# Kernel optimization log

Hardware: AMD Instinct MI355X
Metric: run time of the kernel (lower is better)

## Reference

```python
import jax, jax.numpy as jnp
import numpy as np

N, NOBJ, M, H, W = 512, 16, 8192, 128, 128


def _rand_rotations(key, n):
    A = jax.random.normal(key, (n, 3, 3), dtype=jnp.float32)
    q, r = jnp.linalg.qr(A)
    q = q * jnp.sign(jnp.diagonal(r, axis1=-2, axis2=-1))[:, None, :]
    det = jnp.linalg.det(q)  # +-1; flip first column if det == -1
    q = q.at[:, :, 0].multiply(det[:, None])
    return q


def setup_inputs() -> dict:
    key = jax.random.key(0)
    ks = jax.random.split(key, 10)
    obj_id = jax.random.randint(ks[0], (N,), 0, NOBJ, dtype=jnp.int32)
    # realistic pinhole intrinsics (pixels), slight per-sample jitter
    base_K = jnp.array([[600.0, 0.0, 64.0], [0.0, 600.0, 64.0], [0.0, 0.0, 1.0]], jnp.float32)
    cam_K = base_K[None] + jax.random.normal(ks[1], (N, 3, 3)) * jnp.array(
        [[5.0, 0.0, 1.0], [0.0, 5.0, 1.0], [0.0, 0.0, 0.0]], jnp.float32)
    gt_R = _rand_rotations(ks[2], N)
    # small rotational perturbation for pred
    pred_R = _rand_rotations(ks[3], N) @ gt_R
    gt_t = jnp.concatenate([jax.random.normal(ks[4], (N, 2)) * 20.0,
                            500.0 + jax.random.uniform(ks[4], (N, 1)) * 300.0], axis=-1)
    pred_t = gt_t + jax.random.normal(ks[5], (N, 3)) * 5.0
    mesh_points = jax.random.normal(ks[6], (NOBJ, M, 3)) * 50.0  # mm-scale meshes
    diameters = 150.0 + jax.random.uniform(ks[7], (NOBJ,)) * 150.0
    gt_coord_3d_roi = jax.random.normal(ks[8], (N, 3, H, W)) * 50.0
    gt_mask_vis_roi = jax.random.bernoulli(ks[9], 0.4, (N, 1, H, W))
    return dict(obj_id=obj_id, cam_K=cam_K, gt_cam_R_m2c=gt_R, gt_cam_t_m2c=gt_t,
                pred_cam_R_m2c=pred_R, pred_cam_t_m2c=pred_t,
                gt_coord_3d_roi=gt_coord_3d_roi, gt_mask_vis_roi=gt_mask_vis_roi,
                mesh_points=mesh_points, diameters=diameters)


def _project(K, x):
    # K: [N,3,3], x: [N,...,3] -> pixel coords [N,...,2]
    h = jnp.einsum('nij,n...j->n...i', K, x)
    return h[..., :2] / h[..., 2:3]


def reference(obj_id, cam_K, gt_cam_R_m2c, gt_cam_t_m2c, pred_cam_R_m2c,
              pred_cam_t_m2c, gt_coord_3d_roi, gt_mask_vis_roi, mesh_points, diameters):
    # RE (degrees)
    R_diff = pred_cam_R_m2c @ jnp.swapaxes(gt_cam_R_m2c, -2, -1)
    trace = R_diff[..., 0, 0] + R_diff[..., 1, 1] + R_diff[..., 2, 2]
    re = jnp.arccos((jnp.clip(trace, -1.0, 3.0) - 1.0) * 0.5) * (180.0 / jnp.pi)
    # TE (cm)
    te = jnp.linalg.norm(pred_cam_t_m2c - gt_cam_t_m2c, axis=-1) * 100.0
    # ADD: mean distance between transformed mesh points, / diameter
    pts = mesh_points[obj_id]                      # [N,M,3]
    dR = pred_cam_R_m2c - gt_cam_R_m2c
    dt = pred_cam_t_m2c - gt_cam_t_m2c
    diff = jnp.einsum('nij,nmj->nmi', dR, pts) + dt[:, None, :]
    ad = jnp.linalg.norm(diff, axis=-1).mean(axis=-1) / diameters[obj_id]
    # PROJ: mean projected distance over mesh points
    xp = jnp.einsum('nij,nmj->nmi', pred_cam_R_m2c, pts) + pred_cam_t_m2c[:, None, :]
    xg = jnp.einsum('nij,nmj->nmi', gt_cam_R_m2c, pts) + gt_cam_t_m2c[:, None, :]
    pj = jnp.linalg.norm(_project(cam_K, xp) - _project(cam_K, xg), axis=-1).mean(axis=-1)
    # PROJ-visible: same over visible ROI pixels (masked mean instead of ragged gather)
    verts = jnp.transpose(gt_coord_3d_roi, (0, 2, 3, 1))  # [N,H,W,3]
    vp = jnp.einsum('nij,nhwj->nhwi', pred_cam_R_m2c, verts) + pred_cam_t_m2c[:, None, None, :]
    vg = jnp.einsum('nij,nhwj->nhwi', gt_cam_R_m2c, verts) + gt_cam_t_m2c[:, None, None, :]
    d = jnp.linalg.norm(_project(cam_K, vp) - _project(cam_K, vg), axis=-1)  # [N,H,W]
    mask = gt_mask_vis_roi[:, 0].astype(d.dtype)
    pv = (d * mask).sum(axis=(1, 2)) / jnp.maximum(mask.sum(axis=(1, 2)), 1.0)
    return re, te, ad, pj, pv
```

## Files before the change

### kernel.cpp

```cpp
#include <hip/hip_runtime.h>
#include <math.h>

#define NS    512
#define NOBJ  16
#define MPTS  8192
#define HH    128
#define WW    128
#define HW    (HH * WW)
#define BLOCK 512
#define NWAVE (BLOCK / 64)
#define P_IT  (HW / 4 / BLOCK)
#define M_IT  (MPTS / 4 / BLOCK)

typedef float f4 __attribute__((ext_vector_type(4)));
typedef int   i4 __attribute__((ext_vector_type(4)));

__device__ __forceinline__ float frcp(float x)  { return __builtin_amdgcn_rcpf(x); }
__device__ __forceinline__ float fsqrt(float x) { return __builtin_amdgcn_sqrtf(x); }
__device__ __forceinline__ float rfl(float x) {
    return __int_as_float(__builtin_amdgcn_readfirstlane(__float_as_int(x)));
}
__device__ __forceinline__ void sched_fence() {
#if __has_builtin(__builtin_amdgcn_sched_barrier)
    __builtin_amdgcn_sched_barrier(0);
#endif
}
__device__ __forceinline__ f4 ntl_f4(const f4* p) {
#if __has_builtin(__builtin_nontemporal_load)
    return __builtin_nontemporal_load(p);
#else
    return *p;
#endif
}
__device__ __forceinline__ i4 ntl_i4(const i4* p) {
#if __has_builtin(__builtin_nontemporal_load)
    return __builtin_nontemporal_load(p);
#else
    return *p;
#endif
}

__device__ __forceinline__ void fuse_proj(const float* __restrict__ cam_K,
                                          const float* __restrict__ R,
                                          const float* __restrict__ t, int n,
                                          float A[9], float b[3]) {
    float K[9], Rr[9], tt[3];
#pragma unroll
    for (int i = 0; i < 9; ++i) { K[i] = cam_K[n * 9 + i]; Rr[i] = R[n * 9 + i]; }
#pragma unroll
    for (int i = 0; i < 3; ++i) tt[i] = t[n * 3 + i];
#pragma unroll
    for (int r = 0; r < 3; ++r) {
#pragma unroll
        for (int c = 0; c < 3; ++c)
            A[r * 3 + c] = rfl(K[r * 3 + 0] * Rr[0 * 3 + c]
                             + K[r * 3 + 1] * Rr[1 * 3 + c]
                             + K[r * 3 + 2] * Rr[2 * 3 + c]);
        b[r] = rfl(K[r * 3 + 0] * tt[0] + K[r * 3 + 1] * tt[1] + K[r * 3 + 2] * tt[2]);
    }
}

__global__ __attribute__((amdgpu_flat_work_group_size(BLOCK, BLOCK),
                          amdgpu_waves_per_eu(4, 4)))
void score_kernel(
    const int*   __restrict__ obj_id,
    const float* __restrict__ cam_K,
    const float* __restrict__ gt_R,
    const float* __restrict__ gt_t,
    const float* __restrict__ pr_R,
    const float* __restrict__ pr_t,
    const float* __restrict__ coord,
    const int*   __restrict__ mask,
    const float* __restrict__ mesh,
    const float* __restrict__ diam,
    float*       __restrict__ out)
{
    const int n   = blockIdx.x;
    const int tid = threadIdx.x;

    float Ap[9], Ag[9], bp[3], bg[3], dR[9], dt[3];
    fuse_proj(cam_K, pr_R, pr_t, n, Ap, bp);
    fuse_proj(cam_K, gt_R, gt_t, n, Ag, bg);
#pragma unroll
    for (int i = 0; i < 9; ++i) dR[i] = rfl(pr_R[n * 9 + i] - gt_R[n * 9 + i]);
#pragma unroll
    for (int i = 0; i < 3; ++i) dt[i] = rfl(pr_t[n * 3 + i] - gt_t[n * 3 + i]);
    const int obj = __builtin_amdgcn_readfirstlane(obj_id[n]);

    const float* cx = coord + (size_t)n * 3 * HW;
    const f4* cx4 = (const f4*)cx;
    const f4* cy4 = (const f4*)(cx + HW);
    const f4* cz4 = (const f4*)(cx + 2 * HW);
    const i4* mk4 = (const i4*)(mask + (size_t)n * HW);

    f4 AX[4], AY[4], AZ[4];
    i4 AM[4];
#pragma unroll
    for (int t = 0; t < 3; ++t) {
        const int p = t * BLOCK + tid;
        AX[t] = ntl_f4(cx4 + p);
        AY[t] = ntl_f4(cy4 + p);
        AZ[t] = ntl_f4(cz4 + p);
        AM[t] = ntl_i4(mk4 + p);
    }

    float s_pv = 0.0f, s_m = 0.0f;
#pragma unroll
    for (int it = 0; it < P_IT; ++it) {
        if (it + 3 < P_IT) {
            const int t = it + 3;
            const int s = t & 3;
            const int p = t * BLOCK + tid;
            AX[s] = ntl_f4(cx4 + p);
            AY[s] = ntl_f4(cy4 + p);
            AZ[s] = ntl_f4(cz4 + p);
            AM[s] = ntl_i4(mk4 + p);
        }
        sched_fence();
        const int s = it & 3;
        const float xs[4] = {AX[s].x, AX[s].y, AX[s].z, AX[s].w};
        const float ys[4] = {AY[s].x, AY[s].y, AY[s].z, AY[s].w};
        const float zs[4] = {AZ[s].x, AZ[s].y, AZ[s].z, AZ[s].w};
        const int   ms[4] = {AM[s].x, AM[s].y, AM[s].z, AM[s].w};
#pragma unroll
        for (int j = 0; j < 4; ++j) {
            const float x = xs[j], y = ys[j], z = zs[j];
            const float hpx = fmaf(Ap[0], x, fmaf(Ap[1], y, fmaf(Ap[2], z, bp[0])));
            const float hpy = fmaf(Ap[3], x, fmaf(Ap[4], y, fmaf(Ap[5], z, bp[1])));
            const float hpz = fmaf(Ap[6], x, fmaf(Ap[7], y, fmaf(Ap[8], z, bp[2])));
            const float hgx = fmaf(Ag[0], x, fmaf(Ag[1], y, fmaf(Ag[2], z, bg[0])));
            const float hgy = fmaf(Ag[3], x, fmaf(Ag[4], y, fmaf(Ag[5], z, bg[1])));
            const float hgz = fmaf(Ag[6], x, fmaf(Ag[7], y, fmaf(Ag[8], z, bg[2])));
            const float iwp = frcp(hpz), iwg = frcp(hgz);
            const float du = fmaf(hpx, iwp, -hgx * iwg);
            const float dv = fmaf(hpy, iwp, -hgy * iwg);
            const float d  = fsqrt(fmaf(du, du, dv * dv));
            const float fm = (ms[j] != 0) ? 1.0f : 0.0f;
            s_pv += d * fm;
            s_m  += fm;
        }
    }

    const f4* mp4 = (const f4*)(mesh + (size_t)obj * MPTS * 3);
    f4 MF[M_IT][3];
#pragma unroll
    for (int it = 0; it < M_IT; ++it) {
        const int k = it * BLOCK + tid;
        MF[it][0] = mp4[k * 3 + 0];
        MF[it][1] = mp4[k * 3 + 1];
        MF[it][2] = mp4[k * 3 + 2];
    }
    sched_fence();

    float s_ad = 0.0f, s_pj = 0.0f;
#pragma unroll
    for (int it = 0; it < M_IT; ++it) {
        const f4 f0 = MF[it][0], f1 = MF[it][1], f2 = MF[it][2];
        const float px[4] = {f0.x, f0.w, f1.z, f2.y};
        const float py[4] = {f0.y, f1.x, f1.w, f2.z};
        const float pz[4] = {f0.z, f1.y, f2.x, f2.w};
#pragma unroll
        for (int j = 0; j < 4; ++j) {
            const float x = px[j], y = py[j], z = pz[j];
            const float dx = fmaf(dR[0], x, fmaf(dR[1], y, fmaf(dR[2], z, dt[0])));
            const float dy = fmaf(dR[3], x, fmaf(dR[4], y, fmaf(dR[5], z, dt[1])));
            const float dz = fmaf(dR[6], x, fmaf(dR[7], y, fmaf(dR[8], z, dt[2])));
            s_ad += fsqrt(fmaf(dx, dx, fmaf(dy, dy, dz * dz)));
            const float hpx = fmaf(Ap[0], x, fmaf(Ap[1], y, fmaf(Ap[2], z, bp[0])));
            const float hpy = fmaf(Ap[3], x, fmaf(Ap[4], y, fmaf(Ap[5], z, bp[1])));
            const float hpz = fmaf(Ap[6], x, fmaf(Ap[7], y, fmaf(Ap[8], z, bp[2])));
            const float hgx = fmaf(Ag[0], x, fmaf(Ag[1], y, fmaf(Ag[2], z, bg[0])));
            const float hgy = fmaf(Ag[3], x, fmaf(Ag[4], y, fmaf(Ag[5], z, bg[1])));
            const float hgz = fmaf(Ag[6], x, fmaf(Ag[7], y, fmaf(Ag[8], z, bg[2])));
            const float iwp = frcp(hpz), iwg = frcp(hgz);
            const float du = fmaf(hpx, iwp, -hgx * iwg);
            const float dv = fmaf(hpy, iwp, -hgy * iwg);
            s_pj += fsqrt(fmaf(du, du, dv * dv));
        }
    }

    float vals[4] = {s_ad, s_pj, s_pv, s_m};
#pragma unroll
    for (int k = 0; k < 4; ++k)
#pragma unroll
        for (int off = 32; off > 0; off >>= 1)
            vals[k] += __shfl_down(vals[k], off, 64);

    __shared__ float red[4][NWAVE];
    const int wave = tid >> 6, lane = tid & 63;
    if (lane == 0) {
#pragma unroll
        for (int k = 0; k < 4; ++k) red[k][wave] = vals[k];
    }
    __syncthreads();

    if (tid == 0) {
        float tot[4];
#pragma unroll
        for (int k = 0; k < 4; ++k) {
            float s = 0.0f;
#pragma unroll
            for (int w = 0; w < NWAVE; ++w) s += red[k][w];
            tot[k] = s;
        }
        float Rg9[9], Rp9[9];
#pragma unroll
        for (int i = 0; i < 9; ++i) { Rg9[i] = gt_R[n * 9 + i]; Rp9[i] = pr_R[n * 9 + i]; }
        float trace = 0.0f;
#pragma unroll
        for (int i = 0; i < 9; ++i) trace += Rp9[i] * Rg9[i];
        trace = fminf(fmaxf(trace, -1.0f), 3.0f);
        const float te = sqrtf(dt[0] * dt[0] + dt[1] * dt[1] + dt[2] * dt[2]) * 100.0f;

        out[0 * NS + n] = acosf((trace - 1.0f) * 0.5f) * (180.0f / 3.14159265358979323846f);
        out[1 * NS + n] = te;
        out[2 * NS + n] = tot[0] * (1.0f / MPTS) / diam[obj];
        out[3 * NS + n] = tot[1] * (1.0f / MPTS);
        out[4 * NS + n] = tot[2] / fmaxf(tot[3], 1.0f);
    }
}

extern "C" void kernel_launch(void* const* d_in, const int* in_sizes, int n_in,
                              void* d_out, int out_size, void* d_ws, size_t ws_size,
                              hipStream_t stream) {
    const int*   obj_id = (const int*)  d_in[0];
    const float* cam_K  = (const float*)d_in[1];
    const float* gt_R   = (const float*)d_in[2];
    const float* gt_t   = (const float*)d_in[3];
    const float* pr_R   = (const float*)d_in[4];
    const float* pr_t   = (const float*)d_in[5];
    const float* coord  = (const float*)d_in[6];
    const int*   mask   = (const int*)  d_in[7];
    const float* mesh   = (const float*)d_in[8];
    const float* diam   = (const float*)d_in[9];
    float* out = (float*)d_out;

    score_kernel<<<NS, BLOCK, 0, stream>>>(obj_id, cam_K, gt_R, gt_t, pr_R, pr_t,
                                           coord, mask, mesh, diam, out);
}
```

Baseline: 184.4 us.

## Give each wave a contiguous pixel span with double-buffered two-group load stages

Rewrites the visible-pixel loop so each wave owns a contiguous slice of the ROI and walks it in stages of two 256-element groups. Stages are double-buffered, and the next stage is loaded after computing the current one instead of using a 3-deep rotating prefetch across the whole block. The aim is more sequential, DRAM-page-friendly access per wave and a different balance of loads in flight versus compute. Register use per thread stays about the same (4 groups of x/y/z/mask), though the prefetch distance and stride pattern change.

Result: no change. 182.9 us (-0.8%).

```diff
diff --git a/kernel.cpp b/kernel.cpp
--- a/kernel.cpp
+++ b/kernel.cpp
@@ -9,7 +9,10 @@
 #define HW    (HH * WW)
 #define BLOCK 512
 #define NWAVE (BLOCK / 64)
-#define P_IT  (HW / 4 / BLOCK)
+#define WSPAN (HW / NWAVE)
+#define GRP   256
+#define STG   2
+#define NSTG  (WSPAN / (GRP * STG))
 #define M_IT  (MPTS / 4 / BLOCK)
 
 typedef float f4 __attribute__((ext_vector_type(4)));
@@ -75,8 +78,10 @@
     const float* __restrict__ diam,
     float*       __restrict__ out)
 {
-    const int n   = blockIdx.x;
-    const int tid = threadIdx.x;
+    const int n    = blockIdx.x;
+    const int tid  = threadIdx.x;
+    const int w    = tid >> 6;
+    const int lane = tid & 63;
 
     float Ap[9], Ag[9], bp[3], bg[3], dR[9], dt[3];
     fuse_proj(cam_K, pr_R, pr_t, n, Ap, bp);
@@ -88,56 +93,61 @@
     const int obj = __builtin_amdgcn_readfirstlane(obj_id[n]);
 
     const float* cx = coord + (size_t)n * 3 * HW;
-    const f4* cx4 = (const f4*)cx;
-    const f4* cy4 = (const f4*)(cx + HW);
-    const f4* cz4 = (const f4*)(cx + 2 * HW);
-    const i4* mk4 = (const i4*)(mask + (size_t)n * HW);
-
-    f4 AX[4], AY[4], AZ[4];
-    i4 AM[4];
-#pragma unroll
-    for (int t = 0; t < 3; ++t) {
-        const int p = t * BLOCK + tid;
-        AX[t] = ntl_f4(cx4 + p);
-        AY[t] = ntl_f4(cy4 + p);
-        AZ[t] = ntl_f4(cz4 + p);
-        AM[t] = ntl_i4(mk4 + p);
-    }
+    const float* cy = cx + HW;
+    const float* cz = cx + 2 * HW;
+    const int*   mk = mask + (size_t)n * HW;
+    const int wbase = w * WSPAN + 4 * lane;
+
+    f4 X[2][STG], Y[2][STG], Z[2][STG];
+    i4 Mq[2][STG];
+
+#define LOAD_STAGE(s, b)                                                     \
+    {                                                                        \
+        _Pragma("unroll")                                                    \
+        for (int g = 0; g < STG; ++g) {                                      \
+            const int p = wbase + (s) * (STG * GRP) + g * GRP;               \
+            X[b][g]  = ntl_f4((const f4*)(cx + p));                          \
+            Y[b][g]  = ntl_f4((const f4*)(cy + p));                          \
+            Z[b][g]  = ntl_f4((const f4*)(cz + p));                          \
+            Mq[b][g] = ntl_i4((const i4*)(mk + p));                          \
+        }                                                                    \
+    }
+
+    LOAD_STAGE(0, 0)
+    LOAD_STAGE(1, 1)
+    sched_fence();
 
     float s_pv = 0.0f, s_m = 0.0f;
 #pragma unroll
-    for (int it = 0; it < P_IT; ++it) {
-        if (it + 3 < P_IT) {
-            const int t = it + 3;
-            const int s = t & 3;
-            const int p = t * BLOCK + tid;
-            AX[s] = ntl_f4(cx4 + p);
-            AY[s] = ntl_f4(cy4 + p);
-            AZ[s] = ntl_f4(cz4 + p);
-            AM[s] = ntl_i4(mk4 + p);
-        }
-        sched_fence();
-        const int s = it & 3;
-        const float xs[4] = {AX[s].x, AX[s].y, AX[s].z, AX[s].w};
-        const float ys[4] = {AY[s].x, AY[s].y, AY[s].z, AY[s].w};
-        const float zs[4] = {AZ[s].x, AZ[s].y, AZ[s].z, AZ[s].w};
-        const int   ms[4] = {AM[s].x, AM[s].y, AM[s].z, AM[s].w};
-#pragma unroll
-        for (int j = 0; j < 4; ++j) {
-            const float x = xs[j], y = ys[j], z = zs[j];
-            const float hpx = fmaf(Ap[0], x, fmaf(Ap[1], y, fmaf(Ap[2], z, bp[0])));
-            const float hpy = fmaf(Ap[3], x, fmaf(Ap[4], y, fmaf(Ap[5], z, bp[1])));
-            const float hpz = fmaf(Ap[6], x, fmaf(Ap[7], y, fmaf(Ap[8], z, bp[2])));
-            const float hgx = fmaf(Ag[0], x, fmaf(Ag[1], y, fmaf(Ag[2], z, bg[0])));
-            const float hgy = fmaf(Ag[3], x, fmaf(Ag[4], y, fmaf(Ag[5], z, bg[1])));
-            const float hgz = fmaf(Ag[6], x, fmaf(Ag[7], y, fmaf(Ag[8], z, bg[2])));
-            const float iwp = frcp(hpz), iwg = frcp(hgz);
-            const float du = fmaf(hpx, iwp, -hgx * iwg);
-            const float dv = fmaf(hpy, iwp, -hgy * iwg);
-            const float d  = fsqrt(fmaf(du, du, dv * dv));
-            const float fm = (ms[j] != 0) ? 1.0f : 0.0f;
-            s_pv += d * fm;
-            s_m  += fm;
+    for (int s = 0; s < NSTG; ++s) {
+        const int b = s & 1;
+#pragma unroll
+        for (int g = 0; g < STG; ++g) {
+            const float xs[4] = {X[b][g].x, X[b][g].y, X[b][g].z, X[b][g].w};
+            const float ys[4] = {Y[b][g].x, Y[b][g].y, Y[b][g].z, Y[b][g].w};
+            const float zs[4] = {Z[b][g].x, Z[b][g].y, Z[b][g].z, Z[b][g].w};
+            const int   ms[4] = {Mq[b][g].x, Mq[b][g].y, Mq[b][g].z, Mq[b][g].w};
+#pragma unroll
+            for (int j = 0; j < 4; ++j) {
+                const float x = xs[j], y = ys[j], z = zs[j];
+                const float hpx = fmaf(Ap[0], x, fmaf(Ap[1], y, fmaf(Ap[2], z, bp[0])));
+                const float hpy = fmaf(Ap[3], x, fmaf(Ap[4], y, fmaf(Ap[5], z, bp[1])));
+                const float hpz = fmaf(Ap[6], x, fmaf(Ap[7], y, fmaf(Ap[8], z, bp[2])));
+                const float hgx = fmaf(Ag[0], x, fmaf(Ag[1], y, fmaf(Ag[2], z, bg[0])));
+                const float hgy = fmaf(Ag[3], x, fmaf(Ag[4], y, fmaf(Ag[5], z, bg[1])));
+                const float hgz = fmaf(Ag[6], x, fmaf(Ag[7], y, fmaf(Ag[8], z, bg[2])));
+                const float iwp = frcp(hpz), iwg = frcp(hgz);
+                const float du = fmaf(hpx, iwp, -hgx * iwg);
+                const float dv = fmaf(hpy, iwp, -hgy * iwg);
+                const float d  = fsqrt(fmaf(du, du, dv * dv));
+                const float fm = (ms[j] != 0) ? 1.0f : 0.0f;
+                s_pv += d * fm;
+                s_m  += fm;
+            }
+        }
+        if (s + 2 < NSTG) {
+            LOAD_STAGE(s + 2, b)
+            sched_fence();
         }
     }
 
@@ -187,10 +197,9 @@
             vals[k] += __shfl_down(vals[k], off, 64);
 
     __shared__ float red[4][NWAVE];
-    const int wave = tid >> 6, lane = tid & 63;
     if (lane == 0) {
 #pragma unroll
-        for (int k = 0; k < 4; ++k) red[k][wave] = vals[k];
+        for (int k = 0; k < 4; ++k) red[k][w] = vals[k];
     }
     __syncthreads();
 
@@ -200,7 +209,7 @@
         for (int k = 0; k < 4; ++k) {
             float s = 0.0f;
 #pragma unroll
-            for (int w = 0; w < NWAVE; ++w) s += red[k][w];
+            for (int wv = 0; wv < NWAVE; ++wv) s += red[k][wv];
             tot[k] = s;
         }
         float Rg9[9], Rp9[9];
```
